# Performance work log

Measured on AMD Instinct MI355X. Metric: run time of the kernel, lower is better.

Reference implementation:

```python
import jax, jax.numpy as jnp
import numpy as np

VOCAB = 38
EMB = 128
CTX = 5  # context window size
HIDDEN = [512, 256, 128]


def setup_inputs() -> dict:
    key = jax.random.key(0)
    ks = jax.random.split(key, 16)
    B, S = 64, 1024
    encrypted_input = jax.random.randint(ks[0], (B, S), 0, VOCAB, dtype=jnp.int32)
    # embedding table, uniform(-0.1, 0.1), padding_idx=0 row zeroed
    emb = jax.random.uniform(ks[1], (VOCAB, EMB), jnp.float32, -0.1, 0.1)
    emb = emb.at[0].set(0.0)
    dims = [EMB * CTX] + HIDDEN + [VOCAB]
    params = {}
    for i in range(len(dims) - 1):
        fan_in, fan_out = dims[i], dims[i + 1]
        limit = float(np.sqrt(6.0 / (fan_in + fan_out)))  # xavier uniform
        params[f"W{i+1}"] = jax.random.uniform(ks[2 + i], (fan_out, fan_in), jnp.float32, -limit, limit)
        params[f"b{i+1}"] = jnp.zeros((fan_out,), jnp.float32)
    return {"encrypted_input": encrypted_input, "emb": emb, **params}


def reference(encrypted_input, emb, W1, b1, W2, b2, W3, b3, W4, b4):
    B, S = encrypted_input.shape
    pad = CTX // 2
    x = emb[encrypted_input]                                   # [B, S, E]
    xp = jnp.pad(x, ((0, 0), (pad, pad), (0, 0)))              # [B, S+4, E]
    # sliding window of CTX tokens, flattened -> [B, S, CTX*E]
    ctx = jnp.concatenate([xp[:, i:i + S, :] for i in range(CTX)], axis=-1)
    h = ctx.reshape(B * S, CTX * EMB)                          # fused batched GEMM rows
    h = jax.nn.relu(h @ W1.T + b1)
    h = jax.nn.relu(h @ W2.T + b2)
    h = jax.nn.relu(h @ W3.T + b3)
    out = h @ W4.T + b4                                        # [B*S, VOCAB]
    return out.reshape(B, S, VOCAB)
```

## Files before the change

kernel.cpp:

```cpp
#include <hip/hip_runtime.h>
#include <hip/hip_bf16.h>

#define SEQ 1024

typedef __attribute__((ext_vector_type(8))) short s16x8;
typedef __attribute__((ext_vector_type(4))) float f32x4;
typedef __attribute__((ext_vector_type(2))) unsigned int u32x2;
typedef __attribute__((ext_vector_type(4))) unsigned int u32x4;
typedef __attribute__((ext_vector_type(2))) float f32x2;

#define GT  0
#define W2P (5 * 39 * 512)
#define W3P (W2P + 256 * 512)
#define W4P (W3P + 64 * 512)

#define F2 (16 * 16)
#define F3 (8 * 8)
#define F4 (3 * 4)
#define FTOT (F2 + F3 + F4)

__device__ __forceinline__ unsigned int f2bf(float f) {
    unsigned int u = __float_as_uint(f);
    return (u + 0x7fffu + ((u >> 16) & 1u)) >> 16;
}

__device__ __forceinline__ unsigned short bfbits(float f) {
    __hip_bfloat16 h = __float2bfloat16(f);
    unsigned short u;
    __builtin_memcpy(&u, &h, 2);
    return u;
}

__device__ __forceinline__ unsigned pk2(float a, float b) {
    return (unsigned)bfbits(a) | ((unsigned)bfbits(b) << 16);
}

__device__ __forceinline__ float bf2f(short x) {
    return __uint_as_float(((unsigned)(unsigned short)x) << 16);
}

__device__ __forceinline__ void cvt8(const s16x8 g, f32x2 o[4]) {
    #pragma unroll
    for (int h = 0; h < 4; ++h) {
        o[h][0] = bf2f(g[2 * h]);
        o[h][1] = bf2f(g[2 * h + 1]);
    }
}

__global__ void prep(const float* __restrict__ w1, const float* __restrict__ w2,
                     const float* __restrict__ w3, const float* __restrict__ w4,
                     const float* __restrict__ emb, const float* __restrict__ b1,
                     unsigned short* __restrict__ dst) {
    if (blockIdx.x < 195) {
        const int j = blockIdx.x / 39;
        const int v = blockIdx.x % 39;
        const int o = threadIdx.x;
        if (v >= 38) {
            dst[GT + (j * 39 + v) * 512 + o] = (j == 0) ? bfbits(b1[o]) : (unsigned short)0;
            return;
        }
        __shared__ float ev[128];
        if (threadIdx.x < 128) ev[threadIdx.x] = emb[v * 128 + threadIdx.x];
        __syncthreads();
        const float* wr = w1 + o * 640 + j * 128;
        float s = (j == 0) ? b1[o] : 0.f;
        #pragma unroll
        for (int e = 0; e < 128; e += 4) {
            const float4 a = *reinterpret_cast<const float4*>(wr + e);
            s += a.x * ev[e] + a.y * ev[e + 1] + a.z * ev[e + 2] + a.w * ev[e + 3];
        }
        dst[GT + (j * 39 + v) * 512 + o] = bfbits(s);
    } else {
        const int g = (blockIdx.x - 195) * 512 + threadIdx.x;
        if (g >= FTOT * 64) return;
        const int lane = g & 63;
        const int t    = g >> 6;
        const float* w; int K, N, KC, base, tl;
        if (t < F2)           { w = w2; K = 512; N = 256; KC = 16; base = W2P; tl = t; }
        else if (t < F2 + F3) { w = w3; K = 256; N = 128; KC = 8;  base = W3P; tl = t - F2; }
        else                  { w = w4; K = 128; N = 38;  KC = 4;  base = W4P; tl = t - F2 - F3; }
        const int ct  = tl / KC;
        const int kc  = tl - ct * KC;
        const int col = ct * 16 + (lane & 15);
        const int k0  = kc * 32 + (lane >> 4) * 8;
        unsigned short o8[8];
        #pragma unroll
        for (int e = 0; e < 8; ++e)
            o8[e] = (col < N) ? (unsigned short)f2bf(w[col * K + k0 + e]) : (unsigned short)0;
        *reinterpret_cast<s16x8*>(dst + base + (size_t)(tl * 64 + lane) * 8) =
            *reinterpret_cast<s16x8*>(o8);
    }
}

#define BA 0
#define BB 32768

#define SWZ(b, row) ((b) ^ (((row) & 15) << 4))

__device__ __forceinline__ u32x2 pack_relu(f32x4 a, float4 b) {
    u32x2 r;
    r[0] = pk2(fmaxf(a[0] + b.x, 0.f), fmaxf(a[1] + b.y, 0.f));
    r[1] = pk2(fmaxf(a[2] + b.z, 0.f), fmaxf(a[3] + b.w, 0.f));
    return r;
}

__launch_bounds__(512, 4)
__global__ void fused_mlp(const int* __restrict__ tok,
                          const unsigned short* __restrict__ wbf,
                          const float* __restrict__ b2,
                          const float* __restrict__ b3,
                          const float* __restrict__ b4,
                          float* __restrict__ out) {
    __shared__ char smem[65536];
    const int tid  = threadIdx.x;
    const int lane = tid & 63;
    const int wave = tid >> 6;
    const int l15  = lane & 15;
    const int l4   = lane >> 4;
    const int r0   = blockIdx.x * 64;
    const int s0   = r0 & (SEQ - 1);
    const int bat  = r0 >> 10;

    const int p1row = tid >> 3;
    const int p1c   = tid & 7;
    int goff[5];
    #pragma unroll
    for (int j = 0; j < 5; ++j) {
        const int sp = s0 - 2 + p1row + j;
        const int t  = (sp >= 0 && sp < SEQ) ? tok[bat * SEQ + sp] : 38;
        goff[j] = (j * 39 + t) * 512;
    }

    #pragma unroll
    for (int it = 0; it < 4; ++it) {
        const int c8 = it * 8 + p1c;
        const int d  = c8 * 8;
        s16x8 g[5];
        #pragma unroll
        for (int j = 0; j < 5; ++j)
            g[j] = *reinterpret_cast<const s16x8*>(wbf + GT + goff[j] + d);
        f32x2 s[4];
        cvt8(g[0], s);
        #pragma unroll
        for (int j = 1; j < 5; ++j) {
            f32x2 t[4];
            cvt8(g[j], t);
            #pragma unroll
            for (int h = 0; h < 4; ++h) s[h] += t[h];
        }
        u32x4 wv;
        #pragma unroll
        for (int h = 0; h < 4; ++h)
            wv[h] = pk2(fmaxf(s[h][0], 0.f), fmaxf(s[h][1], 0.f));
        *reinterpret_cast<u32x4*>(smem + BA + SWZ(p1row * 512 + c8 * 16, p1row)) = wv;
    }
    __syncthreads();

    f32x4 acc2[4][2];
    #pragma unroll
    for (int rt = 0; rt < 4; ++rt)
        #pragma unroll
        for (int ct = 0; ct < 2; ++ct) acc2[rt][ct] = (f32x4){0.f, 0.f, 0.f, 0.f};
    {
        #pragma unroll
        for (int it = 0; it < 4; ++it) {
            const int c8 = it * 8 + p1c;
            const int d  = 256 + c8 * 8;
            s16x8 g[5];
            #pragma unroll
            for (int j = 0; j < 5; ++j)
                g[j] = *reinterpret_cast<const s16x8*>(wbf + GT + goff[j] + d);
            f32x2 s[4];
            cvt8(g[0], s);
            #pragma unroll
            for (int j = 1; j < 5; ++j) {
                f32x2 t[4];
                cvt8(g[j], t);
                #pragma unroll
                for (int h = 0; h < 4; ++h) s[h] += t[h];
            }
            u32x4 wv;
            #pragma unroll
            for (int h = 0; h < 4; ++h)
                wv[h] = pk2(fmaxf(s[h][0], 0.f), fmaxf(s[h][1], 0.f));
            *reinterpret_cast<u32x4*>(smem + BB + SWZ(p1row * 512 + c8 * 16, p1row)) = wv;
        }
        for (int ks = 0; ks < 8; ++ks) {
            s16x8 xv[4];
            #pragma unroll
            for (int rt = 0; rt < 4; ++rt) {
                const int row = rt * 16 + l15;
                xv[rt] = *reinterpret_cast<const s16x8*>(
                    smem + BA + SWZ(row * 512 + ks * 64 + l4 * 16, row));
            }
            __builtin_amdgcn_s_setprio(1);
            #pragma unroll
            for (int ct = 0; ct < 2; ++ct) {
                const s16x8 w = *reinterpret_cast<const s16x8*>(
                    wbf + W2P + (((wave * 2 + ct) * 16 + ks) * 64 + lane) * 8);
                #pragma unroll
                for (int rt = 0; rt < 4; ++rt)
                    acc2[rt][ct] = __builtin_amdgcn_mfma_f32_16x16x32_bf16(w, xv[rt], acc2[rt][ct], 0, 0, 0);
            }
            __builtin_amdgcn_s_setprio(0);
        }
    }
    __syncthreads();

    {
        for (int ks = 0; ks < 8; ++ks) {
            s16x8 xv[4];
            #pragma unroll
            for (int rt = 0; rt < 4; ++rt) {
                const int row = rt * 16 + l15;
                xv[rt] = *reinterpret_cast<const s16x8*>(
                    smem + BB + SWZ(row * 512 + ks * 64 + l4 * 16, row));
            }
            __builtin_amdgcn_s_setprio(1);
            #pragma unroll
            for (int ct = 0; ct < 2; ++ct) {
                const s16x8 w = *reinterpret_cast<const s16x8*>(
                    wbf + W2P + (((wave * 2 + ct) * 16 + 8 + ks) * 64 + lane) * 8);
                #pragma unroll
                for (int rt = 0; rt < 4; ++rt)
                    acc2[rt][ct] = __builtin_amdgcn_mfma_f32_16x16x32_bf16(w, xv[rt], acc2[rt][ct], 0, 0, 0);
            }
            __builtin_amdgcn_s_setprio(0);
        }
        #pragma unroll
        for (int ct = 0; ct < 2; ++ct) {
            const int col0 = (wave * 2 + ct) * 16 + l4 * 4;
            const float4 bb = *reinterpret_cast<const float4*>(b2 + col0);
            #pragma unroll
            for (int rt = 0; rt < 4; ++rt) {
                const int row = rt * 16 + l15;
                *reinterpret_cast<u32x2*>(smem + BA + SWZ(row * 512 + col0 * 2, row)) =
                    pack_relu(acc2[rt][ct], bb);
            }
        }
    }
    __syncthreads();

    {
        f32x4 acc[4];
        #pragma unroll
        for (int rt = 0; rt < 4; ++rt) acc[rt] = (f32x4){0.f, 0.f, 0.f, 0.f};
        for (int ks = 0; ks < 8; ++ks) {
            const s16x8 w = *reinterpret_cast<const s16x8*>(
                wbf + W3P + ((wave * 8 + ks) * 64 + lane) * 8);
            s16x8 xv[4];
            #pragma unroll
            for (int rt = 0; rt < 4; ++rt) {
                const int row = rt * 16 + l15;
                xv[rt] = *reinterpret_cast<const s16x8*>(
                    smem + BA + SWZ(row * 512 + ks * 64 + l4 * 16, row));
            }
            __builtin_amdgcn_s_setprio(1);
            #pragma unroll
            for (int rt = 0; rt < 4; ++rt)
                acc[rt] = __builtin_amdgcn_mfma_f32_16x16x32_bf16(w, xv[rt], acc[rt], 0, 0, 0);
            __builtin_amdgcn_s_setprio(0);
        }
        const int col0 = wave * 16 + l4 * 4;
        const float4 bb = *reinterpret_cast<const float4*>(b3 + col0);
        #pragma unroll
        for (int rt = 0; rt < 4; ++rt) {
            const int row = rt * 16 + l15;
            *reinterpret_cast<u32x2*>(smem + BB + SWZ(row * 256 + col0 * 2, row)) =
                pack_relu(acc[rt], bb);
        }
    }
    __syncthreads();

    for (int task = wave; task < 12; task += 8) {
        const int mt = task >> 2;
        const int rt = task & 3;
        f32x4 acc = (f32x4){0.f, 0.f, 0.f, 0.f};
        #pragma unroll
        for (int ks = 0; ks < 4; ++ks) {
            const int row = rt * 16 + l15;
            const s16x8 xv = *reinterpret_cast<const s16x8*>(
                smem + BB + SWZ(row * 256 + ks * 64 + l4 * 16, row));
            const s16x8 w = *reinterpret_cast<const s16x8*>(
                wbf + W4P + ((mt * 4 + ks) * 64 + lane) * 8);
            acc = __builtin_amdgcn_mfma_f32_16x16x32_bf16(w, xv, acc, 0, 0, 0);
        }
        const int rg   = r0 + rt * 16 + l15;
        const int col0 = mt * 16 + l4 * 4;
        #pragma unroll
        for (int h = 0; h < 2; ++h) {
            const int c = col0 + 2 * h;
            if (c < 38) {
                f32x2 v;
                v[0] = acc[2 * h]     + b4[c];
                v[1] = acc[2 * h + 1] + b4[c + 1];
                *reinterpret_cast<f32x2*>(out + rg * 38 + c) = v;
            }
        }
    }
}

extern "C" void kernel_launch(void* const* d_in, const int* in_sizes, int n_in,
                              void* d_out, int out_size, void* d_ws, size_t ws_size,
                              hipStream_t stream) {
    const int*   tok = (const int*)d_in[0];
    const float* emb = (const float*)d_in[1];
    const float* W1  = (const float*)d_in[2];
    const float* b1  = (const float*)d_in[3];
    const float* W2  = (const float*)d_in[4];
    const float* b2  = (const float*)d_in[5];
    const float* W3  = (const float*)d_in[6];
    const float* b3  = (const float*)d_in[7];
    const float* W4  = (const float*)d_in[8];
    const float* b4  = (const float*)d_in[9];
    float* out = (float*)d_out;
    unsigned short* wbf = (unsigned short*)d_ws;

    const int pack_blocks = (FTOT * 64 + 511) / 512;
    prep<<<195 + pack_blocks, 512, 0, stream>>>(W1, W2, W3, W4, emb, b1, wbf);
    fused_mlp<<<1024, 512, 0, stream>>>(tok, wbf, b2, b3, b4, out);
}
```

Baseline: 49.02 us.

## Pipeline layer-1 gather with layer-2 GEMM in quarter chunks, shrink LDS

```diff
diff --git a/kernel.cpp b/kernel.cpp
--- a/kernel.cpp
+++ b/kernel.cpp
@@ -92,8 +92,10 @@
     }
 }
 
-#define BA 0
-#define BB 32768
+#define QB0 0
+#define QB1 16384
+#define H2S 0
+#define H3S 32768
 
 #define SWZ(b, row) ((b) ^ (((row) & 15) << 4))
 
@@ -111,7 +113,7 @@
                           const float* __restrict__ b3,
                           const float* __restrict__ b4,
                           float* __restrict__ out) {
-    __shared__ char smem[65536];
+    __shared__ char smem[49152];
     const int tid  = threadIdx.x;
     const int lane = tid & 63;
     const int wave = tid >> 6;
@@ -131,41 +133,11 @@
         goff[j] = (j * 39 + t) * 512;
     }
 
-    #pragma unroll
-    for (int it = 0; it < 4; ++it) {
-        const int c8 = it * 8 + p1c;
-        const int d  = c8 * 8;
-        s16x8 g[5];
-        #pragma unroll
-        for (int j = 0; j < 5; ++j)
-            g[j] = *reinterpret_cast<const s16x8*>(wbf + GT + goff[j] + d);
-        f32x2 s[4];
-        cvt8(g[0], s);
-        #pragma unroll
-        for (int j = 1; j < 5; ++j) {
-            f32x2 t[4];
-            cvt8(g[j], t);
-            #pragma unroll
-            for (int h = 0; h < 4; ++h) s[h] += t[h];
-        }
-        u32x4 wv;
-        #pragma unroll
-        for (int h = 0; h < 4; ++h)
-            wv[h] = pk2(fmaxf(s[h][0], 0.f), fmaxf(s[h][1], 0.f));
-        *reinterpret_cast<u32x4*>(smem + BA + SWZ(p1row * 512 + c8 * 16, p1row)) = wv;
-    }
-    __syncthreads();
-
-    f32x4 acc2[4][2];
-    #pragma unroll
-    for (int rt = 0; rt < 4; ++rt)
-        #pragma unroll
-        for (int ct = 0; ct < 2; ++ct) acc2[rt][ct] = (f32x4){0.f, 0.f, 0.f, 0.f};
-    {
-        #pragma unroll
-        for (int it = 0; it < 4; ++it) {
+    auto p1q = [&](int q, int buf) {
+        #pragma unroll
+        for (int it = 0; it < 2; ++it) {
             const int c8 = it * 8 + p1c;
-            const int d  = 256 + c8 * 8;
+            const int d  = q * 128 + c8 * 8;
             s16x8 g[5];
             #pragma unroll
             for (int j = 0; j < 5; ++j)
@@ -183,60 +155,61 @@
             #pragma unroll
             for (int h = 0; h < 4; ++h)
                 wv[h] = pk2(fmaxf(s[h][0], 0.f), fmaxf(s[h][1], 0.f));
-            *reinterpret_cast<u32x4*>(smem + BB + SWZ(p1row * 512 + c8 * 16, p1row)) = wv;
-        }
-        for (int ks = 0; ks < 8; ++ks) {
+            *reinterpret_cast<u32x4*>(smem + buf + SWZ(p1row * 256 + c8 * 16, p1row)) = wv;
+        }
+    };
+
+    f32x4 acc2[4][2];
+    #pragma unroll
+    for (int rt = 0; rt < 4; ++rt)
+        #pragma unroll
+        for (int ct = 0; ct < 2; ++ct) acc2[rt][ct] = (f32x4){0.f, 0.f, 0.f, 0.f};
+
+    auto g2q = [&](int q, int buf) {
+        for (int ks = 0; ks < 4; ++ks) {
             s16x8 xv[4];
             #pragma unroll
             for (int rt = 0; rt < 4; ++rt) {
                 const int row = rt * 16 + l15;
                 xv[rt] = *reinterpret_cast<const s16x8*>(
-                    smem + BA + SWZ(row * 512 + ks * 64 + l4 * 16, row));
+                    smem + buf + SWZ(row * 256 + ks * 64 + l4 * 16, row));
             }
             __builtin_amdgcn_s_setprio(1);
             #pragma unroll
             for (int ct = 0; ct < 2; ++ct) {
                 const s16x8 w = *reinterpret_cast<const s16x8*>(
-                    wbf + W2P + (((wave * 2 + ct) * 16 + ks) * 64 + lane) * 8);
+                    wbf + W2P + (((wave * 2 + ct) * 16 + q * 4 + ks) * 64 + lane) * 8);
                 #pragma unroll
                 for (int rt = 0; rt < 4; ++rt)
                     acc2[rt][ct] = __builtin_amdgcn_mfma_f32_16x16x32_bf16(w, xv[rt], acc2[rt][ct], 0, 0, 0);
             }
             __builtin_amdgcn_s_setprio(0);
         }
-    }
-    __syncthreads();
-
-    {
-        for (int ks = 0; ks < 8; ++ks) {
-            s16x8 xv[4];
-            #pragma unroll
-            for (int rt = 0; rt < 4; ++rt) {
-                const int row = rt * 16 + l15;
-                xv[rt] = *reinterpret_cast<const s16x8*>(
-                    smem + BB + SWZ(row * 512 + ks * 64 + l4 * 16, row));
-            }
-            __builtin_amdgcn_s_setprio(1);
-            #pragma unroll
-            for (int ct = 0; ct < 2; ++ct) {
-                const s16x8 w = *reinterpret_cast<const s16x8*>(
-                    wbf + W2P + (((wave * 2 + ct) * 16 + 8 + ks) * 64 + lane) * 8);
-                #pragma unroll
-                for (int rt = 0; rt < 4; ++rt)
-                    acc2[rt][ct] = __builtin_amdgcn_mfma_f32_16x16x32_bf16(w, xv[rt], acc2[rt][ct], 0, 0, 0);
-            }
-            __builtin_amdgcn_s_setprio(0);
-        }
-        #pragma unroll
-        for (int ct = 0; ct < 2; ++ct) {
-            const int col0 = (wave * 2 + ct) * 16 + l4 * 4;
-            const float4 bb = *reinterpret_cast<const float4*>(b2 + col0);
-            #pragma unroll
-            for (int rt = 0; rt < 4; ++rt) {
-                const int row = rt * 16 + l15;
-                *reinterpret_cast<u32x2*>(smem + BA + SWZ(row * 512 + col0 * 2, row)) =
-                    pack_relu(acc2[rt][ct], bb);
-            }
+    };
+
+    p1q(0, QB0);
+    __syncthreads();
+    p1q(1, QB1);
+    g2q(0, QB0);
+    __syncthreads();
+    p1q(2, QB0);
+    g2q(1, QB1);
+    __syncthreads();
+    p1q(3, QB1);
+    g2q(2, QB0);
+    __syncthreads();
+    g2q(3, QB1);
+    __syncthreads();
+
+    #pragma unroll
+    for (int ct = 0; ct < 2; ++ct) {
+        const int col0 = (wave * 2 + ct) * 16 + l4 * 4;
+        const float4 bb = *reinterpret_cast<const float4*>(b2 + col0);
+        #pragma unroll
+        for (int rt = 0; rt < 4; ++rt) {
+            const int row = rt * 16 + l15;
+            *reinterpret_cast<u32x2*>(smem + H2S + SWZ(row * 512 + col0 * 2, row)) =
+                pack_relu(acc2[rt][ct], bb);
         }
     }
     __syncthreads();
@@ -253,7 +226,7 @@
             for (int rt = 0; rt < 4; ++rt) {
                 const int row = rt * 16 + l15;
                 xv[rt] = *reinterpret_cast<const s16x8*>(
-                    smem + BA + SWZ(row * 512 + ks * 64 + l4 * 16, row));
+                    smem + H2S + SWZ(row * 512 + ks * 64 + l4 * 16, row));
             }
             __builtin_amdgcn_s_setprio(1);
             #pragma unroll
@@ -266,7 +239,7 @@
         #pragma unroll
         for (int rt = 0; rt < 4; ++rt) {
             const int row = rt * 16 + l15;
-            *reinterpret_cast<u32x2*>(smem + BB + SWZ(row * 256 + col0 * 2, row)) =
+            *reinterpret_cast<u32x2*>(smem + H3S + SWZ(row * 256 + col0 * 2, row)) =
                 pack_relu(acc[rt], bb);
         }
     }
@@ -280,7 +253,7 @@
         for (int ks = 0; ks < 4; ++ks) {
             const int row = rt * 16 + l15;
             const s16x8 xv = *reinterpret_cast<const s16x8*>(
-                smem + BB + SWZ(row * 256 + ks * 64 + l4 * 16, row));
+                smem + H3S + SWZ(row * 256 + ks * 64 + l4 * 16, row));
             const s16x8 w = *reinterpret_cast<const s16x8*>(
                 wbf + W4P + ((mt * 4 + ks) * 64 + lane) * 8);
             acc = __builtin_amdgcn_mfma_f32_16x16x32_bf16(w, xv, acc, 0, 0, 0);
```

New measurement: 50.09 us. 1.02x slower.
